# Kernel optimization log

Measured on AMD Instinct MI355X. Metric: run time of the kernel, lower is better.

## Reference

```python
import jax, jax.numpy as jnp
import numpy as np

N, E, D, L = 100000, 500000, 128, 5
NUM_ATOM_FEATS, ATOM_VOCAB = 9, 120
NUM_BOND_FEATS, BOND_VOCAB = 3, 8
BN_EPS = 1e-5


def setup_inputs() -> dict:
    key = jax.random.key(0)
    ks = jax.random.split(key, 16)
    inp = {
        "x": jax.random.randint(ks[0], (N, NUM_ATOM_FEATS), 0, ATOM_VOCAB),
        "edge_index": jax.random.randint(ks[1], (2, E), 0, N),
        "edge_attr": jax.random.randint(ks[2], (E, NUM_BOND_FEATS), 0, BOND_VOCAB),
        "edge_weight": jax.random.uniform(ks[3], (E,), dtype=jnp.float32),
        # parameters
        "atom_emb": jax.random.normal(ks[4], (NUM_ATOM_FEATS, ATOM_VOCAB, D), dtype=jnp.float32) * 0.02,
        "bond_emb": jax.random.normal(ks[5], (L, NUM_BOND_FEATS, BOND_VOCAB, D), dtype=jnp.float32) * 0.02,
        "eps": jnp.zeros((L,), dtype=jnp.float32),
        "W1": jax.random.normal(ks[6], (L, D, 2 * D), dtype=jnp.float32) / np.sqrt(D),
        "b1": jnp.zeros((L, 2 * D), dtype=jnp.float32),
        "g1": jnp.ones((L, 2 * D), dtype=jnp.float32),
        "bt1": jnp.zeros((L, 2 * D), dtype=jnp.float32),
        "W2": jax.random.normal(ks[7], (L, 2 * D, D), dtype=jnp.float32) / np.sqrt(2 * D),
        "b2": jnp.zeros((L, D), dtype=jnp.float32),
        "g_out": jnp.ones((L, D), dtype=jnp.float32),
        "bt_out": jnp.zeros((L, D), dtype=jnp.float32),
    }
    return inp


def _batchnorm(h, g, b):
    # training-mode BN over node axis, biased variance (matches torch BN normalization)
    mu = jnp.mean(h, axis=0)
    var = jnp.mean((h - mu) ** 2, axis=0)
    return g * (h - mu) * jax.lax.rsqrt(var + BN_EPS) + b


def reference(x, edge_index, edge_attr, edge_weight,
              atom_emb, bond_emb, eps, W1, b1, g1, bt1, W2, b2, g_out, bt_out):
    # AtomEncoder: sum per-column embedding lookups -> [N, D]
    h = atom_emb[jnp.arange(NUM_ATOM_FEATS)[None, :], x].sum(axis=1)
    src, dst = edge_index[0], edge_index[1]
    ew = edge_weight[:, None]
    for l in range(L):
        # BondEncoder for layer l -> [E, D]
        e = bond_emb[l][jnp.arange(NUM_BOND_FEATS)[None, :], edge_attr].sum(axis=1)
        # message: relu(x_j + edge_emb) * edge_weight ; aggregate: scatter-add at dst
        m = jax.nn.relu(h[src] + e) * ew
        agg = jax.ops.segment_sum(m, dst, num_segments=N)
        z = (1.0 + eps[l]) * h + agg
        # GIN MLP: Linear -> BN -> ReLU -> Linear
        z = jax.nn.relu(_batchnorm(z @ W1[l] + b1[l], g1[l], bt1[l])) @ W2[l] + b2[l]
        # outer BatchNorm; dropout is identity in eval mode
        h_new = _batchnorm(z, g_out[l], bt_out[l])
        h = h_new if l == L - 1 else jax.nn.relu(h_new)
    return h
```

## Files before the change

kernel.cpp:

```cpp
#include <hip/hip_runtime.h>
#include <hip/hip_bf16.h>
#include <hip/hip_fp16.h>

#define NN 100000
#define EE 500000
#define NP 100096

typedef _Float16 f16;
typedef __attribute__((ext_vector_type(8))) _Float16 f16x8;
typedef __attribute__((ext_vector_type(4))) _Float16 f16x4;
typedef __attribute__((ext_vector_type(4))) float f32x4;

static __device__ __forceinline__ f16x8 relu8(f16x8 a) {
#if __has_builtin(__builtin_elementwise_max)
  f16x8 z = {0, 0, 0, 0, 0, 0, 0, 0};
  return __builtin_elementwise_max(a, z);
#else
  f16x8 r;
#pragma unroll
  for (int i = 0; i < 8; ++i) r[i] = (a[i] > (f16)0) ? a[i] : (f16)0;
  return r;
#endif
}

__global__ __launch_bounds__(256) void prep_kernel(const float* __restrict__ W1,
                                                   const float* __restrict__ W2,
                                                   f16* __restrict__ w1f,
                                                   f16* __restrict__ w2f) {
  int gid = blockIdx.x * 256 + threadIdx.x;
  if (gid < 163840) {
    int l = gid / 32768; int rem = gid % 32768;
    int k = rem / 256;   int n = rem % 256;
    int ctg = n >> 4, m = n & 15;
    int c = k >> 5, q = (k >> 3) & 3, e = k & 7;
    int lane = q * 16 + m;
    w1f[l * 32768 + ((ctg * 4 + c) * 64 + lane) * 8 + e] = (f16)W1[gid];
  } else if (gid < 327680) {
    int g = gid - 163840;
    int l = g / 32768; int rem = g % 32768;
    int k = rem / 128; int n = rem % 128;
    int ctg = n >> 4, m = n & 15;
    int c = k >> 5, q = (k >> 3) & 3, e = k & 7;
    int lane = q * 16 + m;
    w2f[l * 32768 + ((ctg * 8 + c) * 64 + lane) * 8 + e] = (f16)W2[g];
  }
}

__global__ __launch_bounds__(256) void bondtab_kernel(const float* __restrict__ bemb,
                                                      f16* __restrict__ tab) {
  int gid = blockIdx.x * 256 + threadIdx.x;
  int l = gid >> 16;
  int rem = gid & 65535;
  int combo = rem >> 7, d = rem & 127;
  int a0 = combo & 7, a1 = (combo >> 3) & 7, a2 = combo >> 6;
  const float* bl = bemb + l * 3072;
  float v = bl[a0 * 128 + d] + bl[1024 + a1 * 128 + d] + bl[2048 + a2 * 128 + d];
  tab[gid] = (f16)v;
}

__global__ __launch_bounds__(256) void zero_deg_kernel(int* __restrict__ deg) {
  int i = blockIdx.x * 256 + threadIdx.x;
  if (i < NN) deg[i] = 0;
}

__global__ __launch_bounds__(256) void hist_kernel(const int* __restrict__ ei, int* __restrict__ deg) {
  int e = blockIdx.x * 256 + threadIdx.x;
  if (e < EE) atomicAdd(&deg[ei[EE + e]], 1);
}

__global__ __launch_bounds__(256) void scan1_kernel(const int* __restrict__ deg,
                                                    int* __restrict__ offs,
                                                    int* __restrict__ bsum) {
  __shared__ int sh[256];
  int b = blockIdx.x, t = threadIdx.x;
  int base = b * 1024 + t * 4;
  int v[4];
  int s = 0;
#pragma unroll
  for (int i = 0; i < 4; ++i) { v[i] = (base + i < NN) ? deg[base + i] : 0; s += v[i]; }
  sh[t] = s;
  __syncthreads();
  for (int off = 1; off < 256; off <<= 1) {
    int x = (t >= off) ? sh[t - off] : 0;
    __syncthreads();
    sh[t] += x;
    __syncthreads();
  }
  int excl = sh[t] - s;
  if (t == 255) bsum[b] = sh[255];
  int run = excl;
#pragma unroll
  for (int i = 0; i < 4; ++i) {
    if (base + i < NN) offs[base + i] = run;
    run += v[i];
  }
}

__global__ void scan2_kernel(int* __restrict__ bsum, int nb) {
  if (threadIdx.x == 0 && blockIdx.x == 0) {
    int run = 0;
    for (int i = 0; i < nb; ++i) { int v = bsum[i]; bsum[i] = run; run += v; }
  }
}

__global__ __launch_bounds__(256) void scan3_kernel(int* __restrict__ offs,
                                                    const int* __restrict__ bsum,
                                                    int* __restrict__ cursor) {
  int i = blockIdx.x * 256 + threadIdx.x;
  if (i < NN) {
    int v = offs[i] + bsum[i >> 10];
    offs[i] = v;
    cursor[i] = v;
  } else if (i == NN) {
    offs[NN] = EE;
  }
}

__global__ __launch_bounds__(256) void scatter_kernel(const int* __restrict__ ei,
                                                      const int* __restrict__ ea,
                                                      const float* __restrict__ ew,
                                                      int* __restrict__ cursor,
                                                      int* __restrict__ pk,
                                                      float* __restrict__ wsrt) {
  int e = blockIdx.x * 256 + threadIdx.x;
  if (e >= EE) return;
  int dst = ei[EE + e];
  int pos = atomicAdd(&cursor[dst], 1);
  int src = ei[e];
  int a0 = ea[e * 3 + 0], a1 = ea[e * 3 + 1], a2 = ea[e * 3 + 2];
  pk[pos] = src | (a0 << 17) | (a1 << 20) | (a2 << 23);
  wsrt[pos] = ew[e];
}

__global__ __launch_bounds__(256) void zero_slices_kernel(float* __restrict__ p) {
  int i = blockIdx.x * 256 + threadIdx.x;
  *(float4*)(p + i * 4) = float4{0.f, 0.f, 0.f, 0.f};
}

__global__ __launch_bounds__(256) void atom_kernel(const int* __restrict__ x,
                                                   const float* __restrict__ aemb,
                                                   f16* __restrict__ hf) {
  int gid = blockIdx.x * 256 + threadIdx.x;
  int n = gid >> 5, qq = gid & 31;
  if (n >= NN) return;
  float4 s = {0.f, 0.f, 0.f, 0.f};
#pragma unroll
  for (int f = 0; f < 9; ++f) {
    int xi = x[n * 9 + f];
    float4 v = *(const float4*)(aemb + (f * 120 + xi) * 128 + qq * 4);
    s.x += v.x; s.y += v.y; s.z += v.z; s.w += v.w;
  }
  f16x4 o;
  o[0] = (f16)s.x; o[1] = (f16)s.y; o[2] = (f16)s.z; o[3] = (f16)s.w;
  *(f16x4*)(hf + (long)n * 128 + qq * 4) = o;
}

__global__ __launch_bounds__(256) void edge_agg_kernel(const int* __restrict__ offs,
                                                       const int* __restrict__ pk,
                                                       const float* __restrict__ wsrt,
                                                       const f16* __restrict__ tab,
                                                       const float* __restrict__ eps,
                                                       const f16* __restrict__ hf,
                                                       f16* __restrict__ zb) {
  int gid = blockIdx.x * 256 + threadIdx.x;
  int n = gid >> 4, d0 = (gid & 15) * 8;
  if (n >= NN) {
    f16x8 z = {0, 0, 0, 0, 0, 0, 0, 0};
    *(f16x8*)(zb + (long)n * 128 + d0) = z;
    return;
  }
  int s0 = offs[n], s1 = offs[n + 1];
  float e1 = 1.f + eps[0];
  f16x8 hn = *(const f16x8*)(hf + (long)n * 128 + d0);
  float acc[8];
#pragma unroll
  for (int i = 0; i < 8; ++i) acc[i] = e1 * (float)hn[i];

  float wA, wB; f16x8 hA, bA, hB, bB;
  if (s0 < s1) {
    int p = pk[s0]; wA = wsrt[s0];
    hA = *(const f16x8*)(hf + (long)(p & 131071) * 128 + d0);
    bA = *(const f16x8*)(tab + ((p >> 17) & 511) * 128 + d0);
  }
  if (s0 + 1 < s1) {
    int p = pk[s0 + 1]; wB = wsrt[s0 + 1];
    hB = *(const f16x8*)(hf + (long)(p & 131071) * 128 + d0);
    bB = *(const f16x8*)(tab + ((p >> 17) & 511) * 128 + d0);
  }
  int e = s0;
  for (; e + 1 < s1; e += 2) {
    {
      f16x8 sm = relu8(hA + bA);
#pragma unroll
      for (int i = 0; i < 8; ++i) acc[i] += (float)sm[i] * wA;
      if (e + 2 < s1) {
        int p = pk[e + 2]; wA = wsrt[e + 2];
        hA = *(const f16x8*)(hf + (long)(p & 131071) * 128 + d0);
        bA = *(const f16x8*)(tab + ((p >> 17) & 511) * 128 + d0);
      }
    }
    {
      f16x8 sm = relu8(hB + bB);
#pragma unroll
      for (int i = 0; i < 8; ++i) acc[i] += (float)sm[i] * wB;
      if (e + 3 < s1) {
        int p = pk[e + 3]; wB = wsrt[e + 3];
        hB = *(const f16x8*)(hf + (long)(p & 131071) * 128 + d0);
        bB = *(const f16x8*)(tab + ((p >> 17) & 511) * 128 + d0);
      }
    }
  }
  if (e < s1) {
    f16x8 sm = relu8(hA + bA);
#pragma unroll
    for (int i = 0; i < 8; ++i) acc[i] += (float)sm[i] * wA;
  }
  f16x8 o;
#pragma unroll
  for (int i = 0; i < 8; ++i) o[i] = (f16)acc[i];
  *(f16x8*)(zb + (long)n * 128 + d0) = o;
}

__global__ __launch_bounds__(256) void edge_agg_bn_kernel(const int* __restrict__ offs,
                                                          const int* __restrict__ pk,
                                                          const float* __restrict__ wsrt,
                                                          const f16* __restrict__ tab,
                                                          const float* __restrict__ eps, int l,
                                                          const f16* __restrict__ t2,
                                                          const float* __restrict__ sum2s,
                                                          const float* __restrict__ sq2s,
                                                          const float* __restrict__ g2,
                                                          const float* __restrict__ bt2,
                                                          float* __restrict__ s1z,
                                                          f16* __restrict__ zb) {
  __shared__ float sc2[128], sh2[128];
  const int tid = threadIdx.x;
  if (tid < 128) {
    float s = 0.f, s2 = 0.f;
#pragma unroll
    for (int k = 0; k < 16; ++k) { s += sum2s[k * 128 + tid]; s2 += sq2s[k * 128 + tid]; }
    float mu = s * (1.f / NN);
    float var = fmaxf(s2 * (1.f / NN) - mu * mu, 0.f);
    float is = rsqrtf(var + 1e-5f);
    float sc = g2[tid] * is;
    sc2[tid] = sc;
    sh2[tid] = bt2[tid] - mu * sc;
  }
  if (blockIdx.x == 0) {
#pragma unroll
    for (int j = 0; j < 8; ++j)
      *(float4*)(s1z + (j * 256 + tid) * 4) = float4{0.f, 0.f, 0.f, 0.f};
  }
  __syncthreads();
  int gid = blockIdx.x * 256 + tid;
  int n = gid >> 4, d0 = (gid & 15) * 8;
  if (n >= NN) {
    f16x8 z = {0, 0, 0, 0, 0, 0, 0, 0};
    *(f16x8*)(zb + (long)n * 128 + d0) = z;
    return;
  }
  float4 svA = *(const float4*)(sc2 + d0), svB = *(const float4*)(sc2 + d0 + 4);
  float4 shA = *(const float4*)(sh2 + d0), shB = *(const float4*)(sh2 + d0 + 4);
  float sv[8] = {svA.x, svA.y, svA.z, svA.w, svB.x, svB.y, svB.z, svB.w};
  float hv[8] = {shA.x, shA.y, shA.z, shA.w, shB.x, shB.y, shB.z, shB.w};
  f16x8 sv8, hv8;
#pragma unroll
  for (int i = 0; i < 8; ++i) { sv8[i] = (f16)sv[i]; hv8[i] = (f16)hv[i]; }

  int s0 = offs[n], s1 = offs[n + 1];
  float e1 = 1.f + eps[l];
  f16x8 hn = *(const f16x8*)(t2 + (long)n * 128 + d0);
  float acc[8];
#pragma unroll
  for (int i = 0; i < 8; ++i)
    acc[i] = e1 * fmaxf((float)hn[i] * sv[i] + hv[i], 0.f);

  float wA, wB; f16x8 hA, bA, hB, bB;
  if (s0 < s1) {
    int p = pk[s0]; wA = wsrt[s0];
    hA = *(const f16x8*)(t2 + (long)(p & 131071) * 128 + d0);
    bA = *(const f16x8*)(tab + ((p >> 17) & 511) * 128 + d0);
  }
  if (s0 + 1 < s1) {
    int p = pk[s0 + 1]; wB = wsrt[s0 + 1];
    hB = *(const f16x8*)(t2 + (long)(p & 131071) * 128 + d0);
    bB = *(const f16x8*)(tab + ((p >> 17) & 511) * 128 + d0);
  }
  int e = s0;
  for (; e + 1 < s1; e += 2) {
    {
      f16x8 y = relu8(hA * sv8 + hv8);
      f16x8 sm = relu8(y + bA);
#pragma unroll
      for (int i = 0; i < 8; ++i) acc[i] += (float)sm[i] * wA;
      if (e + 2 < s1) {
        int p = pk[e + 2]; wA = wsrt[e + 2];
        hA = *(const f16x8*)(t2 + (long)(p & 131071) * 128 + d0);
        bA = *(const f16x8*)(tab + ((p >> 17) & 511) * 128 + d0);
      }
    }
    {
      f16x8 y = relu8(hB * sv8 + hv8);
      f16x8 sm = relu8(y + bB);
#pragma unroll
      for (int i = 0; i < 8; ++i) acc[i] += (float)sm[i] * wB;
      if (e + 3 < s1) {
        int p = pk[e + 3]; wB = wsrt[e + 3];
        hB = *(const f16x8*)(t2 + (long)(p & 131071) * 128 + d0);
        bB = *(const f16x8*)(tab + ((p >> 17) & 511) * 128 + d0);
      }
    }
  }
  if (e < s1) {
    f16x8 y = relu8(hA * sv8 + hv8);
    f16x8 sm = relu8(y + bA);
#pragma unroll
    for (int i = 0; i < 8; ++i) acc[i] += (float)sm[i] * wA;
  }
  f16x8 o;
#pragma unroll
  for (int i = 0; i < 8; ++i) o[i] = (f16)acc[i];
  *(f16x8*)(zb + (long)n * 128 + d0) = o;
}

__global__ __launch_bounds__(256) void gemm1_kernel(const f16* __restrict__ zb,
                                                    const f16* __restrict__ w1f,
                                                    f16* __restrict__ t1f,
                                                    float* __restrict__ sum1s,
                                                    float* __restrict__ sq1s,
                                                    float* __restrict__ s2z) {
  __shared__ __align__(16) char ldsraw[17408];
  const int tid = threadIdx.x;
  const int lane = tid & 63, w = tid >> 6;
  const int wr = w >> 1, wc = w & 1;
  const int m = lane & 15, q = lane >> 4;
  const int cb = blockIdx.x;
  const int rbase = blockIdx.y * 64;
  const int slice = blockIdx.y & 15;

  if (blockIdx.y == 0 && cb == 0) {
#pragma unroll
    for (int j = 0; j < 4; ++j)
      *(float4*)(s2z + (j * 256 + tid) * 4) = float4{0.f, 0.f, 0.f, 0.f};
  }

  f16x8 B[4][4];
#pragma unroll
  for (int ct = 0; ct < 4; ++ct)
#pragma unroll
    for (int c = 0; c < 4; ++c)
      B[ct][c] = *(const f16x8*)(w1f + (((cb * 8 + wc * 4 + ct) * 4 + c) * 64 + lane) * 8);

  {
    f16x8 st[4];
    const int tofs = tid * 16;
#pragma unroll
    for (int j = 0; j < 4; ++j)
      st[j] = *(const f16x8*)(zb + (long)rbase * 128 + (tofs + j * 4096) / 2);
#pragma unroll
    for (int j = 0; j < 4; ++j) {
      int ofs = tofs + j * 4096;
      int row = ofs >> 8, colb = ofs & 255;
      *(f16x8*)(ldsraw + row * 256 + (colb ^ ((row & 7) << 4))) = st[j];
    }
  }
  __syncthreads();

  f16x8 A[2][4];
#pragma unroll
  for (int rt = 0; rt < 2; ++rt) {
    int row = wr * 32 + rt * 16 + m;
    int rs = row * 256, sw = (row & 7) << 4;
#pragma unroll
    for (int c = 0; c < 4; ++c) {
      int colb = c * 64 + q * 16;
      A[rt][c] = *(const f16x8*)(ldsraw + rs + (colb ^ sw));
    }
  }

  f32x4 acc[2][4];
  const f32x4 zf = {0.f, 0.f, 0.f, 0.f};
#pragma unroll
  for (int a = 0; a < 2; ++a)
#pragma unroll
    for (int b = 0; b < 4; ++b) acc[a][b] = zf;

#pragma unroll
  for (int c = 0; c < 4; ++c)
#pragma unroll
    for (int rt = 0; rt < 2; ++rt)
#pragma unroll
      for (int ct = 0; ct < 4; ++ct)
        acc[rt][ct] = __builtin_amdgcn_mfma_f32_16x16x32_f16(A[rt][c], B[ct][c], acc[rt][ct], 0, 0, 0);

  __syncthreads();
  f16 (*sh)[136] = (f16(*)[136])ldsraw;

#pragma unroll
  for (int ct = 0; ct < 4; ++ct) {
    int lc = wc * 64 + ct * 16 + m;
    int gc = cb * 128 + lc;
    float s = 0.f, s2 = 0.f;
#pragma unroll
    for (int rt = 0; rt < 2; ++rt) {
      int lr = wr * 32 + rt * 16 + q * 4;
#pragma unroll
      for (int i = 0; i < 4; ++i) {
        float v = acc[rt][ct][i];
        s += v; s2 += v * v;
        sh[lr + i][lc] = (f16)v;
      }
    }
    s  += __shfl_xor(s, 16);  s  += __shfl_xor(s, 32);
    s2 += __shfl_xor(s2, 16); s2 += __shfl_xor(s2, 32);
    if (q == 0) {
      unsafeAtomicAdd(&sum1s[slice * 256 + gc], s);
      unsafeAtomicAdd(&sq1s[slice * 256 + gc], s2);
    }
  }
  __syncthreads();
  const int colc = tid & 15, r0 = tid >> 4;
#pragma unroll
  for (int j = 0; j < 4; ++j) {
    int r = j * 16 + r0;
    f16x8 v = *(const f16x8*)(&sh[r][colc * 8]);
    *(f16x8*)(t1f + (long)(rbase + r) * 256 + cb * 128 + colc * 8) = v;
  }
}

__global__ __launch_bounds__(256) void gemm2_kernel(const f16* __restrict__ a1,
                                                    const f16* __restrict__ w2f,
                                                    const float* __restrict__ sum1s,
                                                    const float* __restrict__ sq1s,
                                                    const float* __restrict__ g1,
                                                    const float* __restrict__ bt1,
                                                    f16* __restrict__ t2out,
                                                    float* __restrict__ sum2s,
                                                    float* __restrict__ sq2s) {
  __shared__ __align__(16) char ldsraw[34816];
  float* sc1 = (float*)(ldsraw + 32768);
  float* sh1 = (float*)(ldsraw + 33792);
  const int tid = threadIdx.x;
  const int lane = tid & 63, w = tid >> 6;
  const int wr = w >> 1, wc = w & 1;
  const int m = lane & 15, q = lane >> 4;
  const int rbase = blockIdx.x * 64;
  const int slice = blockIdx.x & 15;

  f16x8 st[8];
  const int tofs = tid * 16;
#pragma unroll
  for (int j = 0; j < 8; ++j)
    st[j] = *(const f16x8*)(a1 + (long)rbase * 256 + (tofs + j * 4096) / 2);

  {
    float s = 0.f, s2 = 0.f;
#pragma unroll
    for (int k = 0; k < 16; ++k) { s += sum1s[k * 256 + tid]; s2 += sq1s[k * 256 + tid]; }
    float mu = s * (1.f / NN);
    float var = fmaxf(s2 * (1.f / NN) - mu * mu, 0.f);
    float is = rsqrtf(var + 1e-5f);
    float sc = g1[tid] * is;
    sc1[tid] = sc;
    sh1[tid] = bt1[tid] - mu * sc;
  }
  __syncthreads();

  {
    const int k0 = (tid & 31) * 8;
    float4 sa = *(const float4*)(sc1 + k0);
    float4 sb = *(const float4*)(sc1 + k0 + 4);
    float4 ha = *(const float4*)(sh1 + k0);
    float4 hb = *(const float4*)(sh1 + k0 + 4);
#pragma unroll
    for (int j = 0; j < 8; ++j) {
      int ofs = tofs + j * 4096;
      int row = ofs >> 9, colb = ofs & 511;
      f16x8 u = st[j], o;
      o[0] = (f16)fmaxf((float)u[0] * sa.x + ha.x, 0.f);
      o[1] = (f16)fmaxf((float)u[1] * sa.y + ha.y, 0.f);
      o[2] = (f16)fmaxf((float)u[2] * sa.z + ha.z, 0.f);
      o[3] = (f16)fmaxf((float)u[3] * sa.w + ha.w, 0.f);
      o[4] = (f16)fmaxf((float)u[4] * sb.x + hb.x, 0.f);
      o[5] = (f16)fmaxf((float)u[5] * sb.y + hb.y, 0.f);
      o[6] = (f16)fmaxf((float)u[6] * sb.z + hb.z, 0.f);
      o[7] = (f16)fmaxf((float)u[7] * sb.w + hb.w, 0.f);
      *(f16x8*)(ldsraw + row * 512 + (colb ^ ((row & 7) << 4))) = o;
    }
  }
  __syncthreads();

  f32x4 acc[2][4];
  const f32x4 zf = {0.f, 0.f, 0.f, 0.f};
#pragma unroll
  for (int a = 0; a < 2; ++a)
#pragma unroll
    for (int b = 0; b < 4; ++b) acc[a][b] = zf;

#pragma unroll
  for (int hh = 0; hh < 2; ++hh) {
    f16x8 A[2][4], B[4][4];
#pragma unroll
    for (int rt = 0; rt < 2; ++rt) {
      int row = wr * 32 + rt * 16 + m;
      int rs = row * 512, sw = (row & 7) << 4;
#pragma unroll
      for (int c = 0; c < 4; ++c) {
        int colb = (hh * 4 + c) * 64 + q * 16;
        A[rt][c] = *(const f16x8*)(ldsraw + rs + (colb ^ sw));
      }
    }
#pragma unroll
    for (int ct = 0; ct < 4; ++ct)
#pragma unroll
      for (int c = 0; c < 4; ++c)
        B[ct][c] = *(const f16x8*)(w2f + (((wc * 4 + ct) * 8 + hh * 4 + c) * 64 + lane) * 8);
#pragma unroll
    for (int c = 0; c < 4; ++c)
#pragma unroll
      for (int rt = 0; rt < 2; ++rt)
#pragma unroll
        for (int ct = 0; ct < 4; ++ct)
          acc[rt][ct] = __builtin_amdgcn_mfma_f32_16x16x32_f16(A[rt][c], B[ct][c], acc[rt][ct], 0, 0, 0);
  }

  __syncthreads();
  f16 (*sh)[136] = (f16(*)[136])ldsraw;

#pragma unroll
  for (int ct = 0; ct < 4; ++ct) {
    int gc = wc * 64 + ct * 16 + m;
    float s = 0.f, s2 = 0.f;
#pragma unroll
    for (int rt = 0; rt < 2; ++rt) {
      int grow = rbase + wr * 32 + rt * 16 + q * 4;
      int lr = wr * 32 + rt * 16 + q * 4;
#pragma unroll
      for (int i = 0; i < 4; ++i) {
        float v = acc[rt][ct][i];
        float vv = (grow + i < NN) ? v : 0.f;
        s += vv; s2 += vv * vv;
        sh[lr + i][gc] = (f16)v;
      }
    }
    s  += __shfl_xor(s, 16);  s  += __shfl_xor(s, 32);
    s2 += __shfl_xor(s2, 16); s2 += __shfl_xor(s2, 32);
    if (q == 0) {
      unsafeAtomicAdd(&sum2s[slice * 128 + gc], s);
      unsafeAtomicAdd(&sq2s[slice * 128 + gc], s2);
    }
  }
  __syncthreads();
  const int colc = tid & 15, r0 = tid >> 4;
#pragma unroll
  for (int j = 0; j < 4; ++j) {
    int r = j * 16 + r0;
    f16x8 v = *(const f16x8*)(&sh[r][colc * 8]);
    *(f16x8*)(t2out + (long)(rbase + r) * 128 + colc * 8) = v;
  }
}

__global__ __launch_bounds__(256) void apply_kernel(const f16* __restrict__ t2,
                                                    const float* __restrict__ sum2s,
                                                    const float* __restrict__ sq2s,
                                                    const float* __restrict__ g2,
                                                    const float* __restrict__ bt2,
                                                    float* __restrict__ outp) {
  __shared__ float sc2[128], sh2[128];
  const int tid = threadIdx.x;
  if (tid < 128) {
    float s = 0.f, s2 = 0.f;
#pragma unroll
    for (int k = 0; k < 16; ++k) { s += sum2s[k * 128 + tid]; s2 += sq2s[k * 128 + tid]; }
    float mu = s * (1.f / NN);
    float var = fmaxf(s2 * (1.f / NN) - mu * mu, 0.f);
    float is = rsqrtf(var + 1e-5f);
    float sc = g2[tid] * is;
    sc2[tid] = sc;
    sh2[tid] = bt2[tid] - mu * sc;
  }
  __syncthreads();
  const int rbase = blockIdx.x * 64;
#pragma unroll
  for (int k = 0; k < 4; ++k) {
    int ci = tid + k * 256;
    int r = ci >> 4, c8 = ci & 15;
    int row = rbase + r;
    if (row >= NN) continue;
    f16x8 u = *(const f16x8*)(t2 + (long)row * 128 + c8 * 8);
    float4 sa = *(const float4*)(sc2 + c8 * 8);
    float4 sb = *(const float4*)(sc2 + c8 * 8 + 4);
    float4 ha = *(const float4*)(sh2 + c8 * 8);
    float4 hb = *(const float4*)(sh2 + c8 * 8 + 4);
    float4 o0 = {(float)u[0] * sa.x + ha.x, (float)u[1] * sa.y + ha.y,
                 (float)u[2] * sa.z + ha.z, (float)u[3] * sa.w + ha.w};
    float4 o1 = {(float)u[4] * sb.x + hb.x, (float)u[5] * sb.y + hb.y,
                 (float)u[6] * sb.z + hb.z, (float)u[7] * sb.w + hb.w};
    *(float4*)(outp + (long)row * 128 + c8 * 8) = o0;
    *(float4*)(outp + (long)row * 128 + c8 * 8 + 4) = o1;
  }
}

extern "C" void kernel_launch(void* const* d_in, const int* in_sizes, int n_in,
                              void* d_out, int out_size, void* d_ws, size_t ws_size,
                              hipStream_t stream) {
  (void)in_sizes; (void)n_in; (void)out_size; (void)ws_size;
  const int*   x      = (const int*)d_in[0];
  const int*   ei     = (const int*)d_in[1];
  const int*   ea     = (const int*)d_in[2];
  const float* ew     = (const float*)d_in[3];
  const float* aemb   = (const float*)d_in[4];
  const float* bemb   = (const float*)d_in[5];
  const float* eps    = (const float*)d_in[6];
  const float* W1     = (const float*)d_in[7];
  const float* g1     = (const float*)d_in[9];
  const float* bt1    = (const float*)d_in[10];
  const float* W2     = (const float*)d_in[11];
  const float* g_out  = (const float*)d_in[13];
  const float* bt_out = (const float*)d_in[14];

  float* outp = (float*)d_out;

  char* ws = (char*)d_ws;
  f16*   hf    = (f16*)(ws);
  f16*   zb    = (f16*)(ws + 25624576);
  f16*   t1f   = (f16*)(ws + 51249152);
  f16*   w1f   = (f16*)(ws + 102498304);
  f16*   w2f   = (f16*)(ws + 102825984);
  float* slices= (float*)(ws + 103153664);
  int*   offs  = (int*)(ws + 103202816);
  int*   bsum  = (int*)(ws + 103602848);
  int*   deg   = (int*)(ws + 103603360);
  int*   cursor= (int*)(ws + 104003360);
  f16*   bsumtab = (f16*)(ws + 103603360);
  int*   pk    = (int*)(ws + 104403360);
  float* wsrt  = (float*)(ws + 106403360);

  float* sum1s = slices;
  float* sq1s  = slices + 4096;
  float* sum2s = slices + 8192;
  float* sq2s  = slices + 10240;

  prep_kernel<<<1280, 256, 0, stream>>>(W1, W2, w1f, w2f);
  zero_deg_kernel<<<391, 256, 0, stream>>>(deg);
  hist_kernel<<<1954, 256, 0, stream>>>(ei, deg);
  scan1_kernel<<<98, 256, 0, stream>>>(deg, offs, bsum);
  scan2_kernel<<<1, 64, 0, stream>>>(bsum, 98);
  scan3_kernel<<<392, 256, 0, stream>>>(offs, bsum, cursor);
  scatter_kernel<<<1954, 256, 0, stream>>>(ei, ea, ew, cursor, pk, wsrt);
  bondtab_kernel<<<1280, 256, 0, stream>>>(bemb, bsumtab);
  zero_slices_kernel<<<12, 256, 0, stream>>>(slices);
  atom_kernel<<<12500, 256, 0, stream>>>(x, aemb, hf);

  for (int l = 0; l < 5; ++l) {
    if (l == 0) {
      edge_agg_kernel<<<6256, 256, 0, stream>>>(offs, pk, wsrt, bsumtab, eps, hf, zb);
    } else {
      edge_agg_bn_kernel<<<6256, 256, 0, stream>>>(offs, pk, wsrt, bsumtab + l * 65536, eps, l,
                                                   hf, sum2s, sq2s,
                                                   g_out + (l - 1) * 128, bt_out + (l - 1) * 128,
                                                   sum1s, zb);
    }
    gemm1_kernel<<<dim3(2, 1564), 256, 0, stream>>>(zb, w1f + l * 32768, t1f, sum1s, sq1s, sum2s);
    gemm2_kernel<<<1564, 256, 0, stream>>>(t1f, w2f + l * 32768, sum1s, sq1s,
                                           g1 + l * 256, bt1 + l * 256, hf, sum2s, sq2s);
    if (l == 4)
      apply_kernel<<<1564, 256, 0, stream>>>(hf, sum2s, sq2s, g_out + 512, bt_out + 512, outp);
  }
}
```

Before: 593.2 us.

## Pack edge key and weight, fuse init kernels, compute both gemm1 halves per block

Packs the per-edge source/attribute key and edge weight into one int2 array, so each gathered edge costs a single 8-byte load instead of two separate 4-byte loads. The weight-prep, degree-zeroing and stats-slice zeroing kernels are merged into one init kernel to cut launch count. gemm1 now computes both 128-column halves of its 64-row tile in one block, so the A tile is staged into LDS once instead of once per half, at the cost of half as many blocks, more serial work per block and extra barriers.

```diff
diff --git a/kernel.cpp b/kernel.cpp
--- a/kernel.cpp
+++ b/kernel.cpp
@@ -23,10 +23,12 @@
 #endif
 }
 
-__global__ __launch_bounds__(256) void prep_kernel(const float* __restrict__ W1,
+__global__ __launch_bounds__(256) void init_kernel(const float* __restrict__ W1,
                                                    const float* __restrict__ W2,
                                                    f16* __restrict__ w1f,
-                                                   f16* __restrict__ w2f) {
+                                                   f16* __restrict__ w2f,
+                                                   int* __restrict__ deg,
+                                                   float* __restrict__ slices) {
   int gid = blockIdx.x * 256 + threadIdx.x;
   if (gid < 163840) {
     int l = gid / 32768; int rem = gid % 32768;
@@ -43,6 +45,11 @@
     int c = k >> 5, q = (k >> 3) & 3, e = k & 7;
     int lane = q * 16 + m;
     w2f[l * 32768 + ((ctg * 8 + c) * 64 + lane) * 8 + e] = (f16)W2[g];
+  } else if (gid < 427680) {
+    int i = gid - 327680;
+    if (i < NN) deg[i] = 0;
+  } else if (gid < 439968) {
+    slices[gid - 427680] = 0.f;
   }
 }
 
@@ -58,11 +65,6 @@
   tab[gid] = (f16)v;
 }
 
-__global__ __launch_bounds__(256) void zero_deg_kernel(int* __restrict__ deg) {
-  int i = blockIdx.x * 256 + threadIdx.x;
-  if (i < NN) deg[i] = 0;
-}
-
 __global__ __launch_bounds__(256) void hist_kernel(const int* __restrict__ ei, int* __restrict__ deg) {
   int e = blockIdx.x * 256 + threadIdx.x;
   if (e < EE) atomicAdd(&deg[ei[EE + e]], 1);
@@ -120,21 +122,14 @@
                                                       const int* __restrict__ ea,
                                                       const float* __restrict__ ew,
                                                       int* __restrict__ cursor,
-                                                      int* __restrict__ pk,
-                                                      float* __restrict__ wsrt) {
+                                                      int2* __restrict__ pkw) {
   int e = blockIdx.x * 256 + threadIdx.x;
   if (e >= EE) return;
   int dst = ei[EE + e];
   int pos = atomicAdd(&cursor[dst], 1);
   int src = ei[e];
   int a0 = ea[e * 3 + 0], a1 = ea[e * 3 + 1], a2 = ea[e * 3 + 2];
-  pk[pos] = src | (a0 << 17) | (a1 << 20) | (a2 << 23);
-  wsrt[pos] = ew[e];
-}
-
-__global__ __launch_bounds__(256) void zero_slices_kernel(float* __restrict__ p) {
-  int i = blockIdx.x * 256 + threadIdx.x;
-  *(float4*)(p + i * 4) = float4{0.f, 0.f, 0.f, 0.f};
+  pkw[pos] = make_int2(src | (a0 << 17) | (a1 << 20) | (a2 << 23), __float_as_int(ew[e]));
 }
 
 __global__ __launch_bounds__(256) void atom_kernel(const int* __restrict__ x,
@@ -156,8 +151,7 @@
 }
 
 __global__ __launch_bounds__(256) void edge_agg_kernel(const int* __restrict__ offs,
-                                                       const int* __restrict__ pk,
-                                                       const float* __restrict__ wsrt,
+                                                       const int2* __restrict__ pkw,
                                                        const f16* __restrict__ tab,
                                                        const float* __restrict__ eps,
                                                        const f16* __restrict__ hf,
@@ -178,14 +172,14 @@
 
   float wA, wB; f16x8 hA, bA, hB, bB;
   if (s0 < s1) {
-    int p = pk[s0]; wA = wsrt[s0];
-    hA = *(const f16x8*)(hf + (long)(p & 131071) * 128 + d0);
-    bA = *(const f16x8*)(tab + ((p >> 17) & 511) * 128 + d0);
+    int2 pw = pkw[s0]; wA = __int_as_float(pw.y);
+    hA = *(const f16x8*)(hf + (long)(pw.x & 131071) * 128 + d0);
+    bA = *(const f16x8*)(tab + ((pw.x >> 17) & 511) * 128 + d0);
   }
   if (s0 + 1 < s1) {
-    int p = pk[s0 + 1]; wB = wsrt[s0 + 1];
-    hB = *(const f16x8*)(hf + (long)(p & 131071) * 128 + d0);
-    bB = *(const f16x8*)(tab + ((p >> 17) & 511) * 128 + d0);
+    int2 pw = pkw[s0 + 1]; wB = __int_as_float(pw.y);
+    hB = *(const f16x8*)(hf + (long)(pw.x & 131071) * 128 + d0);
+    bB = *(const f16x8*)(tab + ((pw.x >> 17) & 511) * 128 + d0);
   }
   int e = s0;
   for (; e + 1 < s1; e += 2) {
@@ -194,9 +188,9 @@
 #pragma unroll
       for (int i = 0; i < 8; ++i) acc[i] += (float)sm[i] * wA;
       if (e + 2 < s1) {
-        int p = pk[e + 2]; wA = wsrt[e + 2];
-        hA = *(const f16x8*)(hf + (long)(p & 131071) * 128 + d0);
-        bA = *(const f16x8*)(tab + ((p >> 17) & 511) * 128 + d0);
+        int2 pw = pkw[e + 2]; wA = __int_as_float(pw.y);
+        hA = *(const f16x8*)(hf + (long)(pw.x & 131071) * 128 + d0);
+        bA = *(const f16x8*)(tab + ((pw.x >> 17) & 511) * 128 + d0);
       }
     }
     {
@@ -204,9 +198,9 @@
 #pragma unroll
       for (int i = 0; i < 8; ++i) acc[i] += (float)sm[i] * wB;
       if (e + 3 < s1) {
-        int p = pk[e + 3]; wB = wsrt[e + 3];
-        hB = *(const f16x8*)(hf + (long)(p & 131071) * 128 + d0);
-        bB = *(const f16x8*)(tab + ((p >> 17) & 511) * 128 + d0);
+        int2 pw = pkw[e + 3]; wB = __int_as_float(pw.y);
+        hB = *(const f16x8*)(hf + (long)(pw.x & 131071) * 128 + d0);
+        bB = *(const f16x8*)(tab + ((pw.x >> 17) & 511) * 128 + d0);
       }
     }
   }
@@ -222,8 +216,7 @@
 }
 
 __global__ __launch_bounds__(256) void edge_agg_bn_kernel(const int* __restrict__ offs,
-                                                          const int* __restrict__ pk,
-                                                          const float* __restrict__ wsrt,
+                                                          const int2* __restrict__ pkw,
                                                           const f16* __restrict__ tab,
                                                           const float* __restrict__ eps, int l,
                                                           const f16* __restrict__ t2,
@@ -277,14 +270,14 @@
 
   float wA, wB; f16x8 hA, bA, hB, bB;
   if (s0 < s1) {
-    int p = pk[s0]; wA = wsrt[s0];
-    hA = *(const f16x8*)(t2 + (long)(p & 131071) * 128 + d0);
-    bA = *(const f16x8*)(tab + ((p >> 17) & 511) * 128 + d0);
+    int2 pw = pkw[s0]; wA = __int_as_float(pw.y);
+    hA = *(const f16x8*)(t2 + (long)(pw.x & 131071) * 128 + d0);
+    bA = *(const f16x8*)(tab + ((pw.x >> 17) & 511) * 128 + d0);
   }
   if (s0 + 1 < s1) {
-    int p = pk[s0 + 1]; wB = wsrt[s0 + 1];
-    hB = *(const f16x8*)(t2 + (long)(p & 131071) * 128 + d0);
-    bB = *(const f16x8*)(tab + ((p >> 17) & 511) * 128 + d0);
+    int2 pw = pkw[s0 + 1]; wB = __int_as_float(pw.y);
+    hB = *(const f16x8*)(t2 + (long)(pw.x & 131071) * 128 + d0);
+    bB = *(const f16x8*)(tab + ((pw.x >> 17) & 511) * 128 + d0);
   }
   int e = s0;
   for (; e + 1 < s1; e += 2) {
@@ -294,9 +287,9 @@
 #pragma unroll
       for (int i = 0; i < 8; ++i) acc[i] += (float)sm[i] * wA;
       if (e + 2 < s1) {
-        int p = pk[e + 2]; wA = wsrt[e + 2];
-        hA = *(const f16x8*)(t2 + (long)(p & 131071) * 128 + d0);
-        bA = *(const f16x8*)(tab + ((p >> 17) & 511) * 128 + d0);
+        int2 pw = pkw[e + 2]; wA = __int_as_float(pw.y);
+        hA = *(const f16x8*)(t2 + (long)(pw.x & 131071) * 128 + d0);
+        bA = *(const f16x8*)(tab + ((pw.x >> 17) & 511) * 128 + d0);
       }
     }
     {
@@ -305,9 +298,9 @@
 #pragma unroll
       for (int i = 0; i < 8; ++i) acc[i] += (float)sm[i] * wB;
       if (e + 3 < s1) {
-        int p = pk[e + 3]; wB = wsrt[e + 3];
-        hB = *(const f16x8*)(t2 + (long)(p & 131071) * 128 + d0);
-        bB = *(const f16x8*)(tab + ((p >> 17) & 511) * 128 + d0);
+        int2 pw = pkw[e + 3]; wB = __int_as_float(pw.y);
+        hB = *(const f16x8*)(t2 + (long)(pw.x & 131071) * 128 + d0);
+        bB = *(const f16x8*)(tab + ((pw.x >> 17) & 511) * 128 + d0);
       }
     }
   }
@@ -334,22 +327,14 @@
   const int lane = tid & 63, w = tid >> 6;
   const int wr = w >> 1, wc = w & 1;
   const int m = lane & 15, q = lane >> 4;
-  const int cb = blockIdx.x;
-  const int rbase = blockIdx.y * 64;
-  const int slice = blockIdx.y & 15;
-
-  if (blockIdx.y == 0 && cb == 0) {
+  const int rbase = blockIdx.x * 64;
+  const int slice = blockIdx.x & 15;
+
+  if (blockIdx.x == 0) {
 #pragma unroll
     for (int j = 0; j < 4; ++j)
       *(float4*)(s2z + (j * 256 + tid) * 4) = float4{0.f, 0.f, 0.f, 0.f};
   }
-
-  f16x8 B[4][4];
-#pragma unroll
-  for (int ct = 0; ct < 4; ++ct)
-#pragma unroll
-    for (int c = 0; c < 4; ++c)
-      B[ct][c] = *(const f16x8*)(w1f + (((cb * 8 + wc * 4 + ct) * 4 + c) * 64 + lane) * 8);
 
   {
     f16x8 st[4];
@@ -377,54 +362,64 @@
       A[rt][c] = *(const f16x8*)(ldsraw + rs + (colb ^ sw));
     }
   }
-
-  f32x4 acc[2][4];
-  const f32x4 zf = {0.f, 0.f, 0.f, 0.f};
-#pragma unroll
-  for (int a = 0; a < 2; ++a)
-#pragma unroll
-    for (int b = 0; b < 4; ++b) acc[a][b] = zf;
-
-#pragma unroll
-  for (int c = 0; c < 4; ++c)
-#pragma unroll
-    for (int rt = 0; rt < 2; ++rt)
-#pragma unroll
-      for (int ct = 0; ct < 4; ++ct)
-        acc[rt][ct] = __builtin_amdgcn_mfma_f32_16x16x32_f16(A[rt][c], B[ct][c], acc[rt][ct], 0, 0, 0);
-
-  __syncthreads();
+  __syncthreads();
+
   f16 (*sh)[136] = (f16(*)[136])ldsraw;
-
-#pragma unroll
-  for (int ct = 0; ct < 4; ++ct) {
-    int lc = wc * 64 + ct * 16 + m;
-    int gc = cb * 128 + lc;
-    float s = 0.f, s2 = 0.f;
-#pragma unroll
-    for (int rt = 0; rt < 2; ++rt) {
-      int lr = wr * 32 + rt * 16 + q * 4;
-#pragma unroll
-      for (int i = 0; i < 4; ++i) {
-        float v = acc[rt][ct][i];
-        s += v; s2 += v * v;
-        sh[lr + i][lc] = (f16)v;
-      }
-    }
-    s  += __shfl_xor(s, 16);  s  += __shfl_xor(s, 32);
-    s2 += __shfl_xor(s2, 16); s2 += __shfl_xor(s2, 32);
-    if (q == 0) {
-      unsafeAtomicAdd(&sum1s[slice * 256 + gc], s);
-      unsafeAtomicAdd(&sq1s[slice * 256 + gc], s2);
-    }
-  }
-  __syncthreads();
   const int colc = tid & 15, r0 = tid >> 4;
-#pragma unroll
-  for (int j = 0; j < 4; ++j) {
-    int r = j * 16 + r0;
-    f16x8 v = *(const f16x8*)(&sh[r][colc * 8]);
-    *(f16x8*)(t1f + (long)(rbase + r) * 256 + cb * 128 + colc * 8) = v;
+
+#pragma unroll
+  for (int h = 0; h < 2; ++h) {
+    f16x8 B[4][4];
+#pragma unroll
+    for (int ct = 0; ct < 4; ++ct)
+#pragma unroll
+      for (int c = 0; c < 4; ++c)
+        B[ct][c] = *(const f16x8*)(w1f + (((h * 8 + wc * 4 + ct) * 4 + c) * 64 + lane) * 8);
+
+    f32x4 acc[2][4];
+    const f32x4 zf = {0.f, 0.f, 0.f, 0.f};
+#pragma unroll
+    for (int a = 0; a < 2; ++a)
+#pragma unroll
+      for (int b = 0; b < 4; ++b) acc[a][b] = zf;
+#pragma unroll
+    for (int c = 0; c < 4; ++c)
+#pragma unroll
+      for (int rt = 0; rt < 2; ++rt)
+#pragma unroll
+        for (int ct = 0; ct < 4; ++ct)
+          acc[rt][ct] = __builtin_amdgcn_mfma_f32_16x16x32_f16(A[rt][c], B[ct][c], acc[rt][ct], 0, 0, 0);
+
+#pragma unroll
+    for (int ct = 0; ct < 4; ++ct) {
+      int lc = wc * 64 + ct * 16 + m;
+      int gc = h * 128 + lc;
+      float s = 0.f, s2 = 0.f;
+#pragma unroll
+      for (int rt = 0; rt < 2; ++rt) {
+        int lr = wr * 32 + rt * 16 + q * 4;
+#pragma unroll
+        for (int i = 0; i < 4; ++i) {
+          float v = acc[rt][ct][i];
+          s += v; s2 += v * v;
+          sh[lr + i][lc] = (f16)v;
+        }
+      }
+      s  += __shfl_xor(s, 16);  s  += __shfl_xor(s, 32);
+      s2 += __shfl_xor(s2, 16); s2 += __shfl_xor(s2, 32);
+      if (q == 0) {
+        unsafeAtomicAdd(&sum1s[slice * 256 + gc], s);
+        unsafeAtomicAdd(&sq1s[slice * 256 + gc], s2);
+      }
+    }
+    __syncthreads();
+#pragma unroll
+    for (int j = 0; j < 4; ++j) {
+      int r = j * 16 + r0;
+      f16x8 v = *(const f16x8*)(&sh[r][colc * 8]);
+      *(f16x8*)(t1f + (long)(rbase + r) * 256 + h * 128 + colc * 8) = v;
+    }
+    __syncthreads();
   }
 }
 
@@ -633,35 +628,32 @@
   int*   deg   = (int*)(ws + 103603360);
   int*   cursor= (int*)(ws + 104003360);
   f16*   bsumtab = (f16*)(ws + 103603360);
-  int*   pk    = (int*)(ws + 104403360);
-  float* wsrt  = (float*)(ws + 106403360);
+  int2*  pkw   = (int2*)(ws + 104403360);
 
   float* sum1s = slices;
   float* sq1s  = slices + 4096;
   float* sum2s = slices + 8192;
   float* sq2s  = slices + 10240;
 
-  prep_kernel<<<1280, 256, 0, stream>>>(W1, W2, w1f, w2f);
-  zero_deg_kernel<<<391, 256, 0, stream>>>(deg);
+  init_kernel<<<1719, 256, 0, stream>>>(W1, W2, w1f, w2f, deg, slices);
   hist_kernel<<<1954, 256, 0, stream>>>(ei, deg);
   scan1_kernel<<<98, 256, 0, stream>>>(deg, offs, bsum);
   scan2_kernel<<<1, 64, 0, stream>>>(bsum, 98);
   scan3_kernel<<<392, 256, 0, stream>>>(offs, bsum, cursor);
-  scatter_kernel<<<1954, 256, 0, stream>>>(ei, ea, ew, cursor, pk, wsrt);
+  scatter_kernel<<<1954, 256, 0, stream>>>(ei, ea, ew, cursor, pkw);
   bondtab_kernel<<<1280, 256, 0, stream>>>(bemb, bsumtab);
-  zero_slices_kernel<<<12, 256, 0, stream>>>(slices);
   atom_kernel<<<12500, 256, 0, stream>>>(x, aemb, hf);
 
   for (int l = 0; l < 5; ++l) {
     if (l == 0) {
-      edge_agg_kernel<<<6256, 256, 0, stream>>>(offs, pk, wsrt, bsumtab, eps, hf, zb);
+      edge_agg_kernel<<<6256, 256, 0, stream>>>(offs, pkw, bsumtab, eps, hf, zb);
     } else {
-      edge_agg_bn_kernel<<<6256, 256, 0, stream>>>(offs, pk, wsrt, bsumtab + l * 65536, eps, l,
+      edge_agg_bn_kernel<<<6256, 256, 0, stream>>>(offs, pkw, bsumtab + l * 65536, eps, l,
                                                    hf, sum2s, sq2s,
                                                    g_out + (l - 1) * 128, bt_out + (l - 1) * 128,
                                                    sum1s, zb);
     }
-    gemm1_kernel<<<dim3(2, 1564), 256, 0, stream>>>(zb, w1f + l * 32768, t1f, sum1s, sq1s, sum2s);
+    gemm1_kernel<<<1564, 256, 0, stream>>>(zb, w1f + l * 32768, t1f, sum1s, sq1s, sum2s);
     gemm2_kernel<<<1564, 256, 0, stream>>>(t1f, w2f + l * 32768, sum1s, sq1s,
                                            g1 + l * 256, bt1 + l * 256, hf, sum2s, sq2s);
     if (l == 4)
```

New measurement: 597.1 us. Within noise of the previous version (+0.6%).
